# Performance work log

Hardware: AMD Instinct MI355X
Metric: run time of the kernel (lower is better)

The kernel has to match this reference:

```python
import jax, jax.numpy as jnp
import numpy as np

DIM = 3072
NUM_HEADS = 24
HEAD_DIM = DIM // NUM_HEADS  # 128
EPS = 1e-6


def rms_norm(x, scale):
    # x: (..., D); torch F.rms_norm over last dim
    var = jnp.mean(jnp.square(x), axis=-1, keepdims=True)
    return x * jax.lax.rsqrt(var + EPS) * scale


def apply_rope(xq, xk, freqs_cis):
    # xq, xk: (B, H, L, D); freqs_cis: (1, 1, L, D//2, 2, 2)
    B, H, L, D = xq.shape
    xq_ = xq.astype(jnp.float32).reshape(B, H, L, D // 2, 1, 2)
    xk_ = xk.astype(jnp.float32).reshape(B, H, L, D // 2, 1, 2)
    # (1,1,L,D/2,2) * (B,H,L,D/2,1) broadcast -> (B,H,L,D/2,2)
    xq_out = freqs_cis[..., 0] * xq_[..., 0] + freqs_cis[..., 1] * xq_[..., 1]
    xk_out = freqs_cis[..., 0] * xk_[..., 0] + freqs_cis[..., 1] * xk_[..., 1]
    return xq_out.reshape(B, H, L, D).astype(xq.dtype), xk_out.reshape(B, H, L, D).astype(xk.dtype)


def setup_inputs() -> dict:
    key = jax.random.key(0)
    ks = jax.random.split(key, 7)
    B, L = 1, 2048
    x = jax.random.normal(ks[0], (B, L, DIM), dtype=jnp.float32)
    pe = jax.random.normal(ks[1], (1, 1, L, HEAD_DIM // 2, 2, 2), dtype=jnp.float32)
    # parameters (torch nn.Linear layout: weight is (out, in))
    s = 1.0 / np.sqrt(DIM)
    w_qkv = jax.random.uniform(ks[2], (3 * DIM, DIM), minval=-s, maxval=s, dtype=jnp.float32)
    w_proj = jax.random.uniform(ks[3], (DIM, DIM), minval=-s, maxval=s, dtype=jnp.float32)
    b_proj = jax.random.uniform(ks[4], (DIM,), minval=-s, maxval=s, dtype=jnp.float32)
    q_scale = jnp.ones((HEAD_DIM,), dtype=jnp.float32)
    k_scale = jnp.ones((HEAD_DIM,), dtype=jnp.float32)
    return {"x": x, "pe": pe, "w_qkv": w_qkv, "w_proj": w_proj,
            "b_proj": b_proj, "q_scale": q_scale, "k_scale": k_scale}


def reference(x, pe, w_qkv, w_proj, b_proj, q_scale, k_scale):
    B, L, _ = x.shape
    qkv = x @ w_qkv.T  # (B, L, 3*DIM)
    qkv = qkv.reshape(B, L, 3, NUM_HEADS, HEAD_DIM)
    qkv = jnp.transpose(qkv, (2, 0, 3, 1, 4))  # (3, B, H, L, D)
    q, k, v = qkv[0], qkv[1], qkv[2]
    # QKNorm (RMSNorm over head_dim)
    q = rms_norm(q, q_scale)
    k = rms_norm(k, k_scale)
    # RoPE
    q, k = apply_rope(q, k, pe)
    # SDPA: softmax(q k^T / sqrt(D)) v, non-causal
    scores = jnp.einsum("bhqd,bhkd->bhqk", q, k) / np.sqrt(HEAD_DIM).astype(np.float32)
    attn = jax.nn.softmax(scores, axis=-1)
    out = jnp.einsum("bhqk,bhkd->bhqd", attn, v)  # (B, H, L, D)
    out = jnp.transpose(out, (0, 2, 1, 3)).reshape(B, L, DIM)  # B L (H D)
    return out @ w_proj.T + b_proj
```

## Files before the change

### kernel.cpp

```cpp
#include <hip/hip_runtime.h>
#include <hip/hip_bf16.h>

typedef _Float16 f16;
typedef _Float16 f16x2 __attribute__((ext_vector_type(2)));
typedef _Float16 f16x4 __attribute__((ext_vector_type(4)));
typedef _Float16 f16x8 __attribute__((ext_vector_type(8)));
typedef float f32x4 __attribute__((ext_vector_type(4)));

#define L_SEQ 2048
#define DIM 3072
#define NHEAD 24
#define HDIM 128

__device__ __forceinline__ void gll16(const f16* g, f16* l) {
    __builtin_amdgcn_global_load_lds((const __attribute__((address_space(1))) void*)g,
                                     (__attribute__((address_space(3))) void*)l, 16, 0, 0);
}

__global__ __launch_bounds__(256) void f32_to_f16_kernel(const float* __restrict__ s,
                                                         f16* __restrict__ d, int n4) {
    int i = blockIdx.x * blockDim.x + threadIdx.x;
    int stride = gridDim.x * blockDim.x;
    for (; i < n4; i += stride) {
        float4 v = reinterpret_cast<const float4*>(s)[i];
        f16x4 o = {(f16)v.x, (f16)v.y, (f16)v.z, (f16)v.w};
        reinterpret_cast<f16x4*>(d)[i] = o;
    }
}


#define GEMM_BODY(T, VM, DO_STAGE)                                                      \
    {                                                                                   \
        asm volatile("s_waitcnt vmcnt(" #VM ")" ::: "memory");                          \
        __builtin_amdgcn_s_barrier();                                                   \
        __builtin_amdgcn_sched_barrier(0);                                              \
        const int slot_ = (T) % 3;                                                      \
        f16x8 af[4], bf[4];                                                             \
        _Pragma("unroll") for (int i = 0; i < 4; i++)                                   \
            af[i] = *reinterpret_cast<const f16x8*>(                                    \
                &As[slot_][(wr + i * 16 + laneM) * 32 + fc16]);                         \
        _Pragma("unroll") for (int j = 0; j < 4; j++)                                   \
            bf[j] = *reinterpret_cast<const f16x8*>(                                    \
                &Bs[slot_][(wc + j * 16 + laneM) * 32 + fc16]);                         \
        if (DO_STAGE) {                                                                 \
            const int t2 = (T) + 2;                                                     \
            const int s2 = t2 % 3;                                                      \
            gll16(Asrc0 + t2 * 32, &As[s2][dstoff]);                                    \
            gll16(Asrc1 + t2 * 32, &As[s2][4096 + dstoff]);                             \
            gll16(Bsrc + t2 * 32, &Bs[s2][dstoff]);                                     \
        }                                                                               \
        __builtin_amdgcn_s_setprio(1);                                                  \
        _Pragma("unroll") for (int i = 0; i < 4; i++)                                   \
            _Pragma("unroll") for (int j = 0; j < 4; j++)                               \
                acc[i][j] =                                                             \
                    __builtin_amdgcn_mfma_f32_16x16x32_f16(af[i], bf[j], acc[i][j],     \
                                                           0, 0, 0);                    \
        __builtin_amdgcn_s_setprio(0);                                                  \
    }

template <int MODE>
__global__ __launch_bounds__(512, 4) void rg_gemm(const f16* __restrict__ A,
                                                  const f16* __restrict__ B,
                                                  f16* __restrict__ Cf16,
                                                  float* __restrict__ Cf32,
                                                  const float* __restrict__ bias,
                                                  int M, int N, int K) {
    __shared__ f16 As[3][256 * 32];
    __shared__ f16 Bs[3][128 * 32];
    const int tid = threadIdx.x;
    const int wid = tid >> 6;
    const int lane = tid & 63;
    const int grp = lane >> 4;
    const int laneM = lane & 15;

    const int nwg = gridDim.x * gridDim.y;
    const int orig = blockIdx.y * gridDim.x + blockIdx.x;
    const int wgid = (orig & 7) * (nwg >> 3) + (orig >> 3);
    const int bx = wgid % gridDim.x;
    const int by = wgid / gridDim.x;
    const int m0 = by * 256;
    const int n0 = bx * 128;

    const int wr = (wid >> 1) * 64;
    const int wc = (wid & 1) * 64;
    const int NT = K >> 5;
    const int fc16 = (grp ^ ((laneM >> 1) & 3)) * 8;

    const int srow = tid >> 2;
    const int scol = (((tid & 3) ^ ((tid >> 3) & 3)) << 3);
    const f16* Asrc0 = A + (size_t)(m0 + srow) * K + scol;
    const f16* Asrc1 = A + (size_t)(m0 + 128 + srow) * K + scol;
    const f16* Bsrc = B + (size_t)(n0 + srow) * K + scol;
    const int dstoff = wid * 512;

    const f32x4 vzero = {0.f, 0.f, 0.f, 0.f};
    f32x4 acc[4][4];
#pragma unroll
    for (int i = 0; i < 4; i++)
#pragma unroll
        for (int j = 0; j < 4; j++) acc[i][j] = vzero;

#pragma unroll
    for (int t = 0; t < 2; t++) {
        gll16(Asrc0 + t * 32, &As[t][dstoff]);
        gll16(Asrc1 + t * 32, &As[t][4096 + dstoff]);
        gll16(Bsrc + t * 32, &Bs[t][dstoff]);
    }

    int t = 0;
    for (; t < NT - 2; ++t) GEMM_BODY(t, 3, true);
    GEMM_BODY(t, 3, false); ++t;
    GEMM_BODY(t, 0, false);

#pragma unroll
    for (int i = 0; i < 4; i++)
#pragma unroll
        for (int j = 0; j < 4; j++)
#pragma unroll
            for (int r = 0; r < 4; r++) {
                int row = m0 + wr + i * 16 + grp * 4 + r;
                int col = n0 + wc + j * 16 + laneM;
                float v = acc[i][j][r];
                if (MODE == 0) {
                    Cf16[(size_t)row * N + col] = (f16)v;
                } else {
                    Cf32[(size_t)row * N + col] = v + bias[col];
                }
            }
}

__global__ __launch_bounds__(64) void fuse_qk_kernel(const f16* __restrict__ qkv,
                                                     const float* __restrict__ pe,
                                                     const float* __restrict__ qs,
                                                     const float* __restrict__ ks,
                                                     f16* __restrict__ qb,
                                                     f16* __restrict__ kb) {
    const int l = blockIdx.x;
    const int h = blockIdx.y;
    const int i = threadIdx.x;
    const f16* row = qkv + (size_t)l * (3 * DIM) + h * HDIM;
    f16x2 qp = *reinterpret_cast<const f16x2*>(row + 2 * i);
    f16x2 kp = *reinterpret_cast<const f16x2*>(row + DIM + 2 * i);
    float q0 = (float)qp[0], q1 = (float)qp[1];
    float k0 = (float)kp[0], k1 = (float)kp[1];
    float sq = q0 * q0 + q1 * q1;
    float sk = k0 * k0 + k1 * k1;
#pragma unroll
    for (int off = 1; off < 64; off <<= 1) {
        sq += __shfl_xor(sq, off);
        sk += __shfl_xor(sk, off);
    }
    const float SCALE = 0.08838834764831845f;
    float rq = rsqrtf(sq * (1.0f / 128.0f) + 1e-6f) * SCALE;
    float rk = rsqrtf(sk * (1.0f / 128.0f) + 1e-6f);
    float4 w = *reinterpret_cast<const float4*>(pe + ((size_t)l * 64 + i) * 4);
    float qa = q0 * rq * qs[2 * i];
    float qbv = q1 * rq * qs[2 * i + 1];
    float ka = k0 * rk * ks[2 * i];
    float kbv = k1 * rk * ks[2 * i + 1];
    f16x2 qo = {(f16)(w.x * qa + w.y * qbv), (f16)(w.z * qa + w.w * qbv)};
    f16x2 ko = {(f16)(w.x * ka + w.y * kbv), (f16)(w.z * ka + w.w * kbv)};
    *reinterpret_cast<f16x2*>(qb + ((size_t)h * L_SEQ + l) * HDIM + 2 * i) = qo;
    *reinterpret_cast<f16x2*>(kb + ((size_t)h * L_SEQ + l) * HDIM + 2 * i) = ko;
}

__global__ __launch_bounds__(256) void transpose_v_kernel(const f16* __restrict__ qkv,
                                                          f16* __restrict__ vT) {
    __shared__ f16 tile[32][33];
    const int tx = threadIdx.x & 31;
    const int ty = threadIdx.x >> 5;
    const int c0 = blockIdx.x * 32;
    const int r0 = blockIdx.y * 32;
#pragma unroll
    for (int j = 0; j < 4; j++)
        tile[ty + j * 8][tx] = qkv[(size_t)(r0 + ty + j * 8) * (3 * DIM) + 2 * DIM + c0 + tx];
    __syncthreads();
#pragma unroll
    for (int j = 0; j < 4; j++)
        vT[(size_t)(c0 + ty + j * 8) * L_SEQ + r0 + tx] = tile[tx][ty + j * 8];
}

#define KVBLK 64
#define NSTEP (L_SEQ / KVBLK)

__device__ __forceinline__ void stage_kv(const f16* __restrict__ Kh,
                                         const f16* __restrict__ Vh,
                                         int k0, f16* Kt, f16* Vt, int tid) {
    const int wid = tid >> 6;
    const int krow = tid >> 4;
    const int kcl = (tid & 15) ^ (krow & 7);
    const int vrow = tid >> 3;
    const int vcl = (tid & 7) ^ (vrow & 7);
#pragma unroll
    for (int i = 0; i < 4; i++)
        gll16(Kh + (size_t)(k0 + i * 16 + krow) * HDIM + kcl * 8, Kt + i * 2048 + wid * 512);
#pragma unroll
    for (int i = 0; i < 4; i++)
        gll16(Vh + (size_t)(i * 32 + vrow) * L_SEQ + k0 + vcl * 8, Vt + i * 2048 + wid * 512);
}

__global__ __launch_bounds__(256, 2) void attn_kernel(const f16* __restrict__ qb,
                                                      const f16* __restrict__ kb,
                                                      const f16* __restrict__ vT,
                                                      f16* __restrict__ attnb) {
    __shared__ f16 Kt[2][64 * 128];
    __shared__ f16 Vt[2][128 * 64];
    __shared__ f16 Pl[4][16 * 72];
    const int tid = threadIdx.x;
    const int wid = tid >> 6;
    const int lane = tid & 63;
    const int grp = lane >> 4;
    const int laneM = lane & 15;
    const int h = blockIdx.y;
    const int q0 = blockIdx.x * 64 + wid * 16;
    const f16* Qh = qb + (size_t)h * L_SEQ * HDIM;
    const f16* Kh = kb + (size_t)h * L_SEQ * HDIM;
    const f16* Vh = vT + (size_t)h * HDIM * L_SEQ;

    f16x8 qf[4];
#pragma unroll
    for (int c = 0; c < 4; c++)
        qf[c] = *reinterpret_cast<const f16x8*>(Qh + (size_t)(q0 + laneM) * HDIM + c * 32 + grp * 8);

    const f32x4 vzero = {0.f, 0.f, 0.f, 0.f};
    f32x4 O[8];
#pragma unroll
    for (int f = 0; f < 8; f++) O[f] = vzero;
    float m = -3.0e38f;
    float lsum = 0.f;
    f16* Prow = &Pl[wid][laneM * 72];
    const int swz = laneM & 7;

    stage_kv(Kh, Vh, 0, Kt[0], Vt[0], tid);

    for (int step = 0; step < NSTEP; ++step) {
        const int cur = step & 1;
        __syncthreads();
        if (step + 1 < NSTEP)
            stage_kv(Kh, Vh, (step + 1) * KVBLK, Kt[cur ^ 1], Vt[cur ^ 1], tid);
        const f16* Kc = Kt[cur];
        const f16* Vc = Vt[cur];

        f32x4 s[4];
#pragma unroll
        for (int cc = 0; cc < 4; cc++) s[cc] = vzero;
#pragma unroll
        for (int cc = 0; cc < 4; cc++) {
            f16x8 kf[4];
#pragma unroll
            for (int c = 0; c < 4; c++)
                kf[c] = *reinterpret_cast<const f16x8*>(
                    &Kc[(cc * 16 + laneM) * 128 + (((c * 4 + grp) ^ swz) * 8)]);
#pragma unroll
            for (int c = 0; c < 4; c++)
                s[cc] = __builtin_amdgcn_mfma_f32_16x16x32_f16(kf[c], qf[c], s[cc], 0, 0, 0);
        }

        float pmax = s[0][0];
#pragma unroll
        for (int cc = 0; cc < 4; cc++)
#pragma unroll
            for (int r = 0; r < 4; r++) pmax = fmaxf(pmax, s[cc][r]);
        if (!__all(pmax <= m + 8.0f)) {
            float pm = fmaxf(pmax, __shfl_xor(pmax, 16));
            pm = fmaxf(pm, __shfl_xor(pm, 32));
            float mnew = fmaxf(m, pm);
            float alpha = __expf(m - mnew);
            m = mnew;
            lsum *= alpha;
            float af[4];
#pragma unroll
            for (int r = 0; r < 4; r++) af[r] = __shfl(alpha, grp * 4 + r);
#pragma unroll
            for (int f = 0; f < 8; f++)
#pragma unroll
                for (int r = 0; r < 4; r++) O[f][r] *= af[r];
        }
        float ps = 0.f;
#pragma unroll
        for (int cc = 0; cc < 4; cc++) {
            f16x4 pk;
#pragma unroll
            for (int r = 0; r < 4; r++) {
                float p = __expf(s[cc][r] - m);
                ps += p;
                pk[r] = (f16)p;
            }
            *reinterpret_cast<f16x4*>(Prow + cc * 16 + grp * 4) = pk;
        }
        ps += __shfl_xor(ps, 16);
        ps += __shfl_xor(ps, 32);
        lsum += ps;

#pragma unroll
        for (int z = 0; z < 2; z++) {
            f16x8 pa = *reinterpret_cast<const f16x8*>(Prow + z * 32 + grp * 8);
#pragma unroll
            for (int f = 0; f < 8; f++) {
                f16x8 vf = *reinterpret_cast<const f16x8*>(
                    &Vc[(f * 16 + laneM) * 64 + (((z * 4 + grp) ^ swz) * 8)]);
                O[f] = __builtin_amdgcn_mfma_f32_16x16x32_f16(pa, vf, O[f], 0, 0, 0);
            }
        }
    }

    float li = 1.0f / lsum;
    float lf[4];
#pragma unroll
    for (int r = 0; r < 4; r++) lf[r] = __shfl(li, grp * 4 + r);
#pragma unroll
    for (int f = 0; f < 8; f++)
#pragma unroll
        for (int r = 0; r < 4; r++) {
            int row = q0 + grp * 4 + r;
            attnb[(size_t)row * DIM + h * HDIM + f * 16 + laneM] = (f16)(O[f][r] * lf[r]);
        }
}

extern "C" void kernel_launch(void* const* d_in, const int* in_sizes, int n_in,
                              void* d_out, int out_size, void* d_ws, size_t ws_size,
                              hipStream_t stream) {
    const float* x = (const float*)d_in[0];
    const float* pe = (const float*)d_in[1];
    const float* w_qkv = (const float*)d_in[2];
    const float* w_proj = (const float*)d_in[3];
    const float* b_proj = (const float*)d_in[4];
    const float* q_scale = (const float*)d_in[5];
    const float* k_scale = (const float*)d_in[6];
    float* out = (float*)d_out;

    char* ws = (char*)d_ws;
    f16* xb     = (f16*)(ws + 0);
    f16* wqkvb  = (f16*)(ws + 12582912);
    f16* wprojb = (f16*)(ws + 69206016);
    f16* qkvb   = (f16*)(ws + 88080384);
    f16* qbuf   = (f16*)(ws + 125829120);
    f16* kbuf   = (f16*)(ws + 138412032);
    f16* vT     = (f16*)(ws + 150994944);
    f16* attnb  = (f16*)(ws + 163577856);
    if (ws_size < 176160768) return;

    f32_to_f16_kernel<<<1024, 256, 0, stream>>>(x, xb, (2048 * 3072) / 4);
    f32_to_f16_kernel<<<2048, 256, 0, stream>>>(w_qkv, wqkvb, (9216 * 3072) / 4);
    f32_to_f16_kernel<<<1024, 256, 0, stream>>>(w_proj, wprojb, (3072 * 3072) / 4);

    rg_gemm<0><<<dim3(72, 8), 512, 0, stream>>>(xb, wqkvb, qkvb, nullptr, nullptr,
                                                2048, 9216, 3072);
    fuse_qk_kernel<<<dim3(2048, 24), 64, 0, stream>>>(qkvb, pe, q_scale, k_scale, qbuf, kbuf);
    transpose_v_kernel<<<dim3(96, 64), 256, 0, stream>>>(qkvb, vT);
    attn_kernel<<<dim3(32, 24), 256, 0, stream>>>(qbuf, kbuf, vT, attnb);
    rg_gemm<1><<<dim3(24, 8), 512, 0, stream>>>(attnb, wprojb, nullptr, out, b_proj,
                                                2048, 3072, 3072);
}
```

Measured before the change: 392.4 us.

## Shrink GEMM tiles, fuse V transpose into QKV epilogue, merge conversion launches

The three fp32-to-fp16 conversions are merged into one launch. The GEMM now uses 128x128 tiles with 256 threads and a column-major tile order, and the QKV GEMM writes V directly in transposed layout, which removes the separate transpose kernel. The QK norm/RoPE kernel now handles four heads per block. The aim is to cut launch overhead and an extra pass over V, and to give the GEMMs more blocks; the cost is more global reloads of A per tile and scattered transposed stores.

```diff
diff --git a/kernel.cpp b/kernel.cpp
--- a/kernel.cpp
+++ b/kernel.cpp
@@ -17,19 +17,30 @@
                                      (__attribute__((address_space(3))) void*)l, 16, 0, 0);
 }
 
-__global__ __launch_bounds__(256) void f32_to_f16_kernel(const float* __restrict__ s,
-                                                         f16* __restrict__ d, int n4) {
+__global__ __launch_bounds__(256) void cvt3_kernel(const float* __restrict__ s0, f16* __restrict__ d0, int n0,
+                                                   const float* __restrict__ s1, f16* __restrict__ d1, int n1,
+                                                   const float* __restrict__ s2, f16* __restrict__ d2, int n2) {
     int i = blockIdx.x * blockDim.x + threadIdx.x;
     int stride = gridDim.x * blockDim.x;
-    for (; i < n4; i += stride) {
-        float4 v = reinterpret_cast<const float4*>(s)[i];
+    for (int j = i; j < n0; j += stride) {
+        float4 v = reinterpret_cast<const float4*>(s0)[j];
         f16x4 o = {(f16)v.x, (f16)v.y, (f16)v.z, (f16)v.w};
-        reinterpret_cast<f16x4*>(d)[i] = o;
-    }
-}
-
-
-#define GEMM_BODY(T, VM, DO_STAGE)                                                      \
+        reinterpret_cast<f16x4*>(d0)[j] = o;
+    }
+    for (int j = i; j < n1; j += stride) {
+        float4 v = reinterpret_cast<const float4*>(s1)[j];
+        f16x4 o = {(f16)v.x, (f16)v.y, (f16)v.z, (f16)v.w};
+        reinterpret_cast<f16x4*>(d1)[j] = o;
+    }
+    for (int j = i; j < n2; j += stride) {
+        float4 v = reinterpret_cast<const float4*>(s2)[j];
+        f16x4 o = {(f16)v.x, (f16)v.y, (f16)v.z, (f16)v.w};
+        reinterpret_cast<f16x4*>(d2)[j] = o;
+    }
+}
+
+
+#define GEMM_BODY_S(T, VM, DO_STAGE)                                                    \
     {                                                                                   \
         asm volatile("s_waitcnt vmcnt(" #VM ")" ::: "memory");                          \
         __builtin_amdgcn_s_barrier();                                                   \
@@ -45,9 +56,10 @@
         if (DO_STAGE) {                                                                 \
             const int t2 = (T) + 2;                                                     \
             const int s2 = t2 % 3;                                                      \
-            gll16(Asrc0 + t2 * 32, &As[s2][dstoff]);                                    \
-            gll16(Asrc1 + t2 * 32, &As[s2][4096 + dstoff]);                             \
+            gll16(Asrc + t2 * 32, &As[s2][dstoff]);                                     \
+            gll16(Asrc + (size_t)64 * K + t2 * 32, &As[s2][2048 + dstoff]);             \
             gll16(Bsrc + t2 * 32, &Bs[s2][dstoff]);                                     \
+            gll16(Bsrc + (size_t)64 * K + t2 * 32, &Bs[s2][2048 + dstoff]);             \
         }                                                                               \
         __builtin_amdgcn_s_setprio(1);                                                  \
         _Pragma("unroll") for (int i = 0; i < 4; i++)                                   \
@@ -59,13 +71,14 @@
     }
 
 template <int MODE>
-__global__ __launch_bounds__(512, 4) void rg_gemm(const f16* __restrict__ A,
-                                                  const f16* __restrict__ B,
-                                                  f16* __restrict__ Cf16,
-                                                  float* __restrict__ Cf32,
-                                                  const float* __restrict__ bias,
-                                                  int M, int N, int K) {
-    __shared__ f16 As[3][256 * 32];
+__global__ __launch_bounds__(256, 4) void rg128_gemm(const f16* __restrict__ A,
+                                                     const f16* __restrict__ B,
+                                                     f16* __restrict__ Cf16,
+                                                     f16* __restrict__ vT,
+                                                     float* __restrict__ Cf32,
+                                                     const float* __restrict__ bias,
+                                                     int M, int N, int K) {
+    __shared__ f16 As[3][128 * 32];
     __shared__ f16 Bs[3][128 * 32];
     const int tid = threadIdx.x;
     const int wid = tid >> 6;
@@ -76,9 +89,9 @@
     const int nwg = gridDim.x * gridDim.y;
     const int orig = blockIdx.y * gridDim.x + blockIdx.x;
     const int wgid = (orig & 7) * (nwg >> 3) + (orig >> 3);
-    const int bx = wgid % gridDim.x;
-    const int by = wgid / gridDim.x;
-    const int m0 = by * 256;
+    const int by = wgid % gridDim.y;
+    const int bx = wgid / gridDim.y;
+    const int m0 = by * 128;
     const int n0 = bx * 128;
 
     const int wr = (wid >> 1) * 64;
@@ -88,8 +101,7 @@
 
     const int srow = tid >> 2;
     const int scol = (((tid & 3) ^ ((tid >> 3) & 3)) << 3);
-    const f16* Asrc0 = A + (size_t)(m0 + srow) * K + scol;
-    const f16* Asrc1 = A + (size_t)(m0 + 128 + srow) * K + scol;
+    const f16* Asrc = A + (size_t)(m0 + srow) * K + scol;
     const f16* Bsrc = B + (size_t)(n0 + srow) * K + scol;
     const int dstoff = wid * 512;
 
@@ -102,42 +114,63 @@
 
 #pragma unroll
     for (int t = 0; t < 2; t++) {
-        gll16(Asrc0 + t * 32, &As[t][dstoff]);
-        gll16(Asrc1 + t * 32, &As[t][4096 + dstoff]);
+        gll16(Asrc + t * 32, &As[t][dstoff]);
+        gll16(Asrc + (size_t)64 * K + t * 32, &As[t][2048 + dstoff]);
         gll16(Bsrc + t * 32, &Bs[t][dstoff]);
+        gll16(Bsrc + (size_t)64 * K + t * 32, &Bs[t][2048 + dstoff]);
     }
 
     int t = 0;
-    for (; t < NT - 2; ++t) GEMM_BODY(t, 3, true);
-    GEMM_BODY(t, 3, false); ++t;
-    GEMM_BODY(t, 0, false);
-
-#pragma unroll
-    for (int i = 0; i < 4; i++)
-#pragma unroll
-        for (int j = 0; j < 4; j++)
-#pragma unroll
-            for (int r = 0; r < 4; r++) {
-                int row = m0 + wr + i * 16 + grp * 4 + r;
-                int col = n0 + wc + j * 16 + laneM;
-                float v = acc[i][j][r];
-                if (MODE == 0) {
-                    Cf16[(size_t)row * N + col] = (f16)v;
-                } else {
-                    Cf32[(size_t)row * N + col] = v + bias[col];
+    for (; t < NT - 2; ++t) GEMM_BODY_S(t, 4, true);
+    GEMM_BODY_S(t, 4, false); ++t;
+    GEMM_BODY_S(t, 0, false);
+
+    if (MODE == 1) {
+#pragma unroll
+        for (int i = 0; i < 4; i++)
+#pragma unroll
+            for (int j = 0; j < 4; j++)
+#pragma unroll
+                for (int r = 0; r < 4; r++) {
+                    int row = m0 + wr + i * 16 + grp * 4 + r;
+                    int col = n0 + wc + j * 16 + laneM;
+                    Cf32[(size_t)row * N + col] = acc[i][j][r] + bias[col];
                 }
+    } else if (n0 < 2 * DIM) {
+#pragma unroll
+        for (int i = 0; i < 4; i++)
+#pragma unroll
+            for (int j = 0; j < 4; j++)
+#pragma unroll
+                for (int r = 0; r < 4; r++) {
+                    int row = m0 + wr + i * 16 + grp * 4 + r;
+                    int col = n0 + wc + j * 16 + laneM;
+                    Cf16[(size_t)row * N + col] = (f16)acc[i][j][r];
+                }
+    } else {
+#pragma unroll
+        for (int i = 0; i < 4; i++)
+#pragma unroll
+            for (int j = 0; j < 4; j++) {
+                int hd = n0 - 2 * DIM + wc + j * 16 + laneM;
+                int row0 = m0 + wr + i * 16 + grp * 4;
+                f16x4 pk;
+#pragma unroll
+                for (int r = 0; r < 4; r++) pk[r] = (f16)acc[i][j][r];
+                *reinterpret_cast<f16x4*>(&vT[(size_t)hd * L_SEQ + row0]) = pk;
             }
-}
-
-__global__ __launch_bounds__(64) void fuse_qk_kernel(const f16* __restrict__ qkv,
-                                                     const float* __restrict__ pe,
-                                                     const float* __restrict__ qs,
-                                                     const float* __restrict__ ks,
-                                                     f16* __restrict__ qb,
-                                                     f16* __restrict__ kb) {
+    }
+}
+
+__global__ __launch_bounds__(256) void fuse_qk_kernel(const f16* __restrict__ qkv,
+                                                      const float* __restrict__ pe,
+                                                      const float* __restrict__ qs,
+                                                      const float* __restrict__ ks,
+                                                      f16* __restrict__ qb,
+                                                      f16* __restrict__ kb) {
     const int l = blockIdx.x;
-    const int h = blockIdx.y;
-    const int i = threadIdx.x;
+    const int h = blockIdx.y * 4 + (threadIdx.x >> 6);
+    const int i = threadIdx.x & 63;
     const f16* row = qkv + (size_t)l * (3 * DIM) + h * HDIM;
     f16x2 qp = *reinterpret_cast<const f16x2*>(row + 2 * i);
     f16x2 kp = *reinterpret_cast<const f16x2*>(row + DIM + 2 * i);
@@ -162,22 +195,6 @@
     f16x2 ko = {(f16)(w.x * ka + w.y * kbv), (f16)(w.z * ka + w.w * kbv)};
     *reinterpret_cast<f16x2*>(qb + ((size_t)h * L_SEQ + l) * HDIM + 2 * i) = qo;
     *reinterpret_cast<f16x2*>(kb + ((size_t)h * L_SEQ + l) * HDIM + 2 * i) = ko;
-}
-
-__global__ __launch_bounds__(256) void transpose_v_kernel(const f16* __restrict__ qkv,
-                                                          f16* __restrict__ vT) {
-    __shared__ f16 tile[32][33];
-    const int tx = threadIdx.x & 31;
-    const int ty = threadIdx.x >> 5;
-    const int c0 = blockIdx.x * 32;
-    const int r0 = blockIdx.y * 32;
-#pragma unroll
-    for (int j = 0; j < 4; j++)
-        tile[ty + j * 8][tx] = qkv[(size_t)(r0 + ty + j * 8) * (3 * DIM) + 2 * DIM + c0 + tx];
-    __syncthreads();
-#pragma unroll
-    for (int j = 0; j < 4; j++)
-        vT[(size_t)(c0 + ty + j * 8) * L_SEQ + r0 + tx] = tile[tx][ty + j * 8];
 }
 
 #define KVBLK 64
@@ -340,15 +357,14 @@
     f16* attnb  = (f16*)(ws + 163577856);
     if (ws_size < 176160768) return;
 
-    f32_to_f16_kernel<<<1024, 256, 0, stream>>>(x, xb, (2048 * 3072) / 4);
-    f32_to_f16_kernel<<<2048, 256, 0, stream>>>(w_qkv, wqkvb, (9216 * 3072) / 4);
-    f32_to_f16_kernel<<<1024, 256, 0, stream>>>(w_proj, wprojb, (3072 * 3072) / 4);
-
-    rg_gemm<0><<<dim3(72, 8), 512, 0, stream>>>(xb, wqkvb, qkvb, nullptr, nullptr,
-                                                2048, 9216, 3072);
-    fuse_qk_kernel<<<dim3(2048, 24), 64, 0, stream>>>(qkvb, pe, q_scale, k_scale, qbuf, kbuf);
-    transpose_v_kernel<<<dim3(96, 64), 256, 0, stream>>>(qkvb, vT);
+    cvt3_kernel<<<2048, 256, 0, stream>>>(x, xb, (2048 * 3072) / 4,
+                                          w_qkv, wqkvb, (9216 * 3072) / 4,
+                                          w_proj, wprojb, (3072 * 3072) / 4);
+
+    rg128_gemm<0><<<dim3(72, 16), 256, 0, stream>>>(xb, wqkvb, qkvb, vT, nullptr, nullptr,
+                                                    2048, 9216, 3072);
+    fuse_qk_kernel<<<dim3(2048, 6), 256, 0, stream>>>(qkvb, pe, q_scale, k_scale, qbuf, kbuf);
     attn_kernel<<<dim3(32, 24), 256, 0, stream>>>(qbuf, kbuf, vT, attnb);
-    rg_gemm<1><<<dim3(24, 8), 512, 0, stream>>>(attnb, wprojb, nullptr, out, b_proj,
-                                                2048, 3072, 3072);
-}
+    rg128_gemm<1><<<dim3(24, 16), 256, 0, stream>>>(attnb, wprojb, nullptr, nullptr, out, b_proj,
+                                                    2048, 3072, 3072);
+}
```

Result: faster. 363.1 us (-7.5%).
